# Kernel optimization log

Hardware: AMD Instinct MI355X
Metric: run time of the kernel (lower is better)

## Reference

```python
import jax, jax.numpy as jnp
import numpy as np

D_MODEL = 512
NHEAD = 8
HEAD_DIM = D_MODEL // NHEAD
SEQ = 4096
BATCH = 2
BASE = 10000.0


def rope_cache(seq_len, dim):
    inv_freq = 1.0 / (BASE ** (jnp.arange(0, dim, 2, dtype=jnp.float32) / dim))
    t = jnp.arange(seq_len, dtype=jnp.float32)
    freqs = jnp.einsum('i,j->ij', t, inv_freq)          # [S, dim/2]
    emb = jnp.concatenate([freqs, freqs], axis=-1)       # [S, dim]
    return jnp.cos(emb), jnp.sin(emb)


def rotate_half(x):
    h = x.shape[-1] // 2
    return jnp.concatenate([-x[..., h:], x[..., :h]], axis=-1)


def setup_inputs() -> dict:
    key = jax.random.key(0)
    ks = jax.random.split(key, 9)
    s = 1.0 / np.sqrt(D_MODEL)
    x = jax.random.normal(ks[0], (BATCH, SEQ, D_MODEL), dtype=jnp.float32)
    Wq = jax.random.uniform(ks[1], (D_MODEL, D_MODEL), jnp.float32, -s, s)
    bq = jax.random.uniform(ks[2], (D_MODEL,), jnp.float32, -s, s)
    Wk = jax.random.uniform(ks[3], (D_MODEL, D_MODEL), jnp.float32, -s, s)
    bk = jax.random.uniform(ks[4], (D_MODEL,), jnp.float32, -s, s)
    Wv = jax.random.uniform(ks[5], (D_MODEL, D_MODEL), jnp.float32, -s, s)
    bv = jax.random.uniform(ks[6], (D_MODEL,), jnp.float32, -s, s)
    Wo = jax.random.uniform(ks[7], (D_MODEL, D_MODEL), jnp.float32, -s, s)
    bo = jax.random.uniform(ks[8], (D_MODEL,), jnp.float32, -s, s)
    # causal mask: True where attention is disallowed (j > i)
    mask = jnp.triu(jnp.ones((SEQ, SEQ), dtype=bool), k=1)
    return {"x": x, "mask": mask, "Wq": Wq, "bq": bq, "Wk": Wk, "bk": bk,
            "Wv": Wv, "bv": bv, "Wo": Wo, "bo": bo}


def reference(x, mask, Wq, bq, Wk, bk, Wv, bv, Wo, bo):
    B, S, _ = x.shape
    def proj(W, b):
        y = x @ W.T + b
        return y.reshape(B, S, NHEAD, HEAD_DIM).transpose(0, 2, 1, 3)  # [B,H,S,D]
    q = proj(Wq, bq)
    k = proj(Wk, bk)
    v = proj(Wv, bv)
    cos, sin = rope_cache(S, HEAD_DIM)                    # [S, D]
    cos = cos[None, None]; sin = sin[None, None]
    q = q * cos + rotate_half(q) * sin
    k = k * cos + rotate_half(k) * sin
    scale = HEAD_DIM ** -0.5
    attn = jnp.einsum('bhid,bhjd->bhij', q, k) * scale    # [B,H,S,S]
    attn = jnp.where(mask[None, None], -jnp.inf, attn)
    attn = jax.nn.softmax(attn, axis=-1)
    out = jnp.einsum('bhij,bhjd->bhid', attn, v)          # [B,H,S,D]
    out = out.transpose(0, 2, 1, 3).reshape(B, S, D_MODEL)
    return out @ Wo.T + bo
```

## Files before the change

### kernel.cpp

```cpp
#include <hip/hip_runtime.h>
#include <hip/hip_bf16.h>

#define SEQLEN 4096
#define DMODEL 512
#define NHEADS 8

typedef short short8 __attribute__((ext_vector_type(8)));
typedef float f32x4  __attribute__((ext_vector_type(4)));
typedef float f32x16 __attribute__((ext_vector_type(16)));
typedef int   int2v  __attribute__((ext_vector_type(2)));

__device__ __forceinline__ unsigned short f2bf(float f) {
    union { float f; unsigned u; } v; v.f = f;
    unsigned r = v.u + 0x7fffu + ((v.u >> 16) & 1u);
    return (unsigned short)(r >> 16);
}
__device__ __forceinline__ float bf2f(unsigned short u) {
    union { unsigned u; float f; } v; v.u = (unsigned)u << 16; return v.f;
}
__device__ __forceinline__ float exp2v(float x) {
    float r; asm("v_exp_f32 %0, %1" : "=v"(r) : "v"(x)); return r;
}
__device__ __forceinline__ unsigned cvtpk(float lo, float hi) {
    unsigned r; asm("v_cvt_pk_bf16_f32 %0, %1, %2" : "=v"(r) : "v"(lo), "v"(hi)); return r;
}
__device__ __forceinline__ int2v pl32(int a, int b) {
    return __builtin_amdgcn_permlane32_swap(a, b, false, false);
}
__device__ __forceinline__ void gload16(const void* g, void* l) {
    __builtin_amdgcn_global_load_lds(
        (const __attribute__((address_space(1))) void*)g,
        (__attribute__((address_space(3))) void*)l, 16, 0, 0);
}
__device__ __forceinline__ int nchunks(int qs) { return (4 * qs + 4 + 9) / 10; }

__global__ __launch_bounds__(256)
void prep_kernel(const float* __restrict__ x,
                 const float* __restrict__ Wq, const float* __restrict__ Wk,
                 const float* __restrict__ Wv, const float* __restrict__ Wo,
                 unsigned short* __restrict__ xb, unsigned short* __restrict__ Wcat,
                 float* __restrict__ ct, float* __restrict__ st) {
    const int gid = blockIdx.x, tid = threadIdx.x;
    if (gid < 4096) {
        int i = gid * 1024 + tid * 4;
        float4 v = *reinterpret_cast<const float4*>(x + i);
        ushort4 o; o.x = f2bf(v.x); o.y = f2bf(v.y); o.z = f2bf(v.z); o.w = f2bf(v.w);
        *reinterpret_cast<ushort4*>(xb + i) = o;
    } else if (gid < 5120) {
        int i = (gid - 4096) * 1024 + tid * 4;
        int z = i >> 18;
        const float* W = (z == 0) ? Wq : (z == 1) ? Wk : (z == 2) ? Wv : Wo;
        int j = i & 262143;
        float4 v = *reinterpret_cast<const float4*>(W + j);
        ushort4 o; o.x = f2bf(v.x); o.y = f2bf(v.y); o.z = f2bf(v.z); o.w = f2bf(v.w);
        *reinterpret_cast<ushort4*>(Wcat + i) = o;
    } else {
        int idx = (gid - 5120) * 256 + tid;
        int s = idx >> 5, f = idx & 31;
        float inv = exp2f((float)f * -0.4152410118609203f);
        float a = (float)s * inv;
        ct[idx] = cosf(a); st[idx] = sinf(a);
    }
}

template<int MODE>
__global__ __launch_bounds__(256)
void gemm_kernel(const unsigned short* __restrict__ A,
                 const unsigned short* __restrict__ W,
                 const float* __restrict__ bq,
                 const float* __restrict__ bk,
                 const float* __restrict__ bv,
                 const float* __restrict__ ctab,
                 const float* __restrict__ stab,
                 unsigned short* __restrict__ Qb,
                 unsigned short* __restrict__ Kb,
                 unsigned short* __restrict__ Vt,
                 float* __restrict__ Fout)
{
    constexpr int K = 512;
    constexpr int BN  = (MODE == 0) ? 128 : 64;
    constexpr int NT  = (MODE == 0) ? 12 : 8;
    constexpr int CPX = (MODE == 0) ? 96 : 64;
    constexpr int NTF = (MODE == 0) ? 4 : 2;
    __shared__ __align__(16) unsigned short a_sh[3][128 * 32];
    __shared__ __align__(16) unsigned short b_sh[3][BN * 32];

    const int raw = blockIdx.x;
    const int bid = (raw & 7) * CPX + (raw >> 3);
    const int bm = bid / NT, bn = bid % NT;
    const int tid = threadIdx.x;
    const int w = tid >> 6, l = tid & 63;
    const int g = l >> 4, l15 = l & 15;
    const int wr = w >> 1, wc = w & 1;

    const int sr0 = tid >> 2;
    const int swzc = (tid & 3) ^ ((sr0 >> 1) & 3);
    const unsigned wbase = (unsigned)(tid & 0xC0) * 16;
    const unsigned short* arow = A + (size_t)(bm * 128 + sr0) * K + swzc * 8;
    const unsigned short* brow = W + (size_t)(bn * BN + sr0) * K + swzc * 8;

    f32x4 acc[4][NTF];
    #pragma unroll
    for (int p = 0; p < 4; ++p)
        #pragma unroll
        for (int q = 0; q < NTF; ++q)
            acc[p][q] = (f32x4){0.f, 0.f, 0.f, 0.f};

    auto stage = [&](int buf, int k0) {
        char* ab = (char*)a_sh[buf];
        char* bb2 = (char*)b_sh[buf];
        gload16(arow + k0,                      ab + wbase);
        gload16(arow + (size_t)64 * K + k0,     ab + 4096 + wbase);
        gload16(brow + k0,                      bb2 + wbase);
        if constexpr (MODE == 0)
            gload16(brow + (size_t)64 * K + k0, bb2 + 4096 + wbase);
    };
    auto waitvm = [&]() {
        if constexpr (MODE == 0) asm volatile("s_waitcnt vmcnt(4)" ::: "memory");
        else                     asm volatile("s_waitcnt vmcnt(3)" ::: "memory");
    };

    stage(0, 0);
    stage(1, 32);
    waitvm();
    __builtin_amdgcn_s_barrier();

    int cb = 0;
    for (int ks = 0; ks < 16; ++ks) {
        int pb = cb + 2; if (pb >= 3) pb -= 3;
        stage(pb, (ks + 2 < 16) ? (ks + 2) * 32 : 480);

        const char* ab = (const char*)a_sh[cb];
        const char* bb2 = (const char*)b_sh[cb];
        short8 af[4], bf[NTF];
        #pragma unroll
        for (int mt = 0; mt < 4; ++mt) {
            int r = wr * 64 + mt * 16 + l15;
            int ofs = (r * 64 + g * 16) ^ (((r >> 1) & 3) << 4);
            af[mt] = *reinterpret_cast<const short8*>(ab + ofs);
        }
        #pragma unroll
        for (int nt = 0; nt < NTF; ++nt) {
            int r = wc * (BN / 2) + nt * 16 + l15;
            int ofs = (r * 64 + g * 16) ^ (((r >> 1) & 3) << 4);
            bf[nt] = *reinterpret_cast<const short8*>(bb2 + ofs);
        }
        __builtin_amdgcn_s_setprio(1);
        #pragma unroll
        for (int mt = 0; mt < 4; ++mt)
            #pragma unroll
            for (int nt = 0; nt < NTF; ++nt)
                acc[mt][nt] = __builtin_amdgcn_mfma_f32_16x16x32_bf16(af[mt], bf[nt], acc[mt][nt], 0, 0, 0);
        __builtin_amdgcn_s_setprio(0);

        waitvm();
        __builtin_amdgcn_s_barrier();
        cb = (cb == 2) ? 0 : cb + 1;
    }

    const int m_base = bm * 128 + wr * 64;

    if (MODE == 1) {
        const int n_base = bn * 64 + wc * 32;
        #pragma unroll
        for (int mt = 0; mt < 4; ++mt)
            for (int nt = 0; nt < NTF; ++nt) {
                int n = n_base + nt * 16 + l15;
                float bb = bq[n];
                #pragma unroll
                for (int i = 0; i < 4; ++i) {
                    int m = m_base + mt * 16 + g * 4 + i;
                    Fout[(size_t)m * 512 + n] = acc[mt][nt][i] + bb;
                }
            }
    } else {
        const int z = bn >> 2;
        const int nc0 = (bn & 3) * 128 + wc * 64;
        const float* bias = (z == 0) ? bq : (z == 1) ? bk : bv;
        if (z < 2) {
            unsigned short* Y = z ? Kb : Qb;
            const float qsc = z ? 1.0f : 0.18033688011112042f;
            #pragma unroll
            for (int mt = 0; mt < 4; ++mt)
                for (int ntl = 0; ntl < 2; ++ntl) {
                    int hd0 = (ntl * 16 + l15) & 31;
                    int n0 = nc0 + ntl * 16 + l15;
                    float bb0 = bias[n0];
                    float bb1 = bias[n0 + 32];
                    #pragma unroll
                    for (int i = 0; i < 4; ++i) {
                        int m = m_base + mt * 16 + g * 4 + i;
                        int sidx = m & (SEQLEN - 1);
                        float cs = ctab[sidx * 32 + hd0];
                        float sn = stab[sidx * 32 + hd0];
                        float v0 = acc[mt][ntl][i] + bb0;
                        float v1 = acc[mt][ntl + 2][i] + bb1;
                        Y[(size_t)m * 512 + n0]      = f2bf((v0 * cs - v1 * sn) * qsc);
                        Y[(size_t)m * 512 + n0 + 32] = f2bf((v1 * cs + v0 * sn) * qsc);
                    }
                }
        } else if constexpr (MODE == 0) {
            asm volatile("s_waitcnt vmcnt(0)" ::: "memory");
            __builtin_amdgcn_s_barrier();
            char* T = (char*)a_sh;
            #pragma unroll
            for (int mt = 0; mt < 4; ++mt)
                #pragma unroll
                for (int nt = 0; nt < 4; ++nt) {
                    int nv_l = wc * 64 + nt * 16 + l15;
                    float bb = bias[(bn & 3) * 128 + nv_l];
                    #pragma unroll
                    for (int i = 0; i < 4; i += 2) {
                        int m_l = wr * 64 + mt * 16 + g * 4 + i;
                        unsigned u = cvtpk(acc[mt][nt][i] + bb, acc[mt][nt][i + 1] + bb);
                        int byte0 = nv_l * 256 + ((m_l * 2) ^ ((nv_l & 7) << 4));
                        *reinterpret_cast<unsigned*>(T + byte0) = u;
                    }
                }
            __builtin_amdgcn_s_barrier();
            const int b_out = bm >> 5;
            const int s0 = (bm & 31) * 128;
            #pragma unroll
            for (int p = 0; p < 8; ++p) {
                int nv_l = p * 16 + (tid >> 4);
                int c = tid & 15;
                int byte = nv_l * 256 + ((c * 16) ^ ((nv_l & 7) << 4));
                short8 v = *reinterpret_cast<const short8*>(T + byte);
                int nv_g = (bn & 3) * 128 + nv_l;
                int hg = nv_g >> 6, d = nv_g & 63;
                *reinterpret_cast<short8*>(
                    Vt + ((size_t)((b_out * 8 + hg) * 64 + d)) * SEQLEN + s0 + c * 8) = v;
            }
        }
    }
}

__global__ __launch_bounds__(256, 2)
void attn_kernel(const unsigned short* __restrict__ Qg,
                 const unsigned short* __restrict__ Kg,
                 const unsigned short* __restrict__ Vt,
                 unsigned short* __restrict__ O,
                 unsigned short* __restrict__ Opt,
                 float* __restrict__ Ml)
{
    __shared__ __align__(16) unsigned short k_sh[3][64 * 64];
    __shared__ __align__(16) unsigned short v_sh[3][64 * 64];

    const int bx = blockIdx.x;
    const int bh = bx & 15;
    const int idx = bx >> 4;
    int qs = 15, accn = 0;
    for (;;) {
        int nb = nchunks(qs);
        if (accn + nb > idx) break;
        accn += nb; --qs;
    }
    const int ck = idx - accn;
    const int HT4 = 4 * qs + 4;
    const int t0 = ck * 10;
    const int t1 = (t0 + 10 < HT4) ? t0 + 10 : HT4;
    const bool single = (HT4 <= 10);
    const int slot = bh * 61 + idx;

    const int b = bh >> 3, hh = bh & 7;
    const int tid = threadIdx.x;
    const int w = tid >> 6, l = tid & 63;
    const int l31 = l & 31, h = l >> 5;

    const size_t qkbase = (size_t)b * SEQLEN * DMODEL + hh * 64;
    const unsigned short* Vrow = Vt + (size_t)bh * 64 * SEQLEN;

    const int r0 = tid >> 3, cb0 = tid & 7;
    const int scs = cb0 ^ (r0 & 7);
    const unsigned short* ksrc0 = Kg + qkbase + (size_t)r0 * DMODEL + scs * 8;
    const unsigned short* vsrc0 = Vrow + (size_t)r0 * SEQLEN + scs * 8;

    const int swz = (l31 & 7) << 4;
    const int td = 4 * qs + w;
    const int tlimit = td + 1;
    const int qg0 = qs * 256 + w * 64 + l31;
    const int qg1 = qg0 + 32;
    const int ql0 = w * 64 + l31;
    const int ql1 = ql0 + 32;

    short8 qf0[4], qf1[4];
    {
        const unsigned short* qr0 = Qg + qkbase + (size_t)qg0 * DMODEL;
        const unsigned short* qr1 = Qg + qkbase + (size_t)qg1 * DMODEL;
        #pragma unroll
        for (int kk = 0; kk < 4; ++kk) {
            qf0[kk] = *reinterpret_cast<const short8*>(qr0 + kk * 16 + h * 8);
            qf1[kk] = *reinterpret_cast<const short8*>(qr1 + kk * 16 + h * 8);
        }
    }

    f32x16 oa00, oa01, oa10, oa11;
    #pragma unroll
    for (int i = 0; i < 16; ++i) { oa00[i] = 0.f; oa01[i] = 0.f; oa10[i] = 0.f; oa11[i] = 0.f; }
    float m0 = -3.0e38f, l0 = 0.f, m1 = -3.0e38f, l1 = 0.f;

    auto stage = [&](int buf, int t) {
        char* kb = (char*)k_sh[buf];
        char* vb = (char*)v_sh[buf];
        const unsigned short* kp = ksrc0 + (size_t)t * 64 * DMODEL;
        const unsigned short* vp = vsrc0 + t * 64;
        gload16(kp,                kb + tid * 16);
        gload16(kp + 32 * DMODEL,  kb + 4096 + tid * 16);
        gload16(vp,                vb + tid * 16);
        gload16(vp + 32 * SEQLEN,  vb + 4096 + tid * 16);
    };

    auto softmax_set = [&](f32x16& sA, f32x16& sB, float& mr, float& lr,
                           f32x16& oaA, f32x16& oaB, short8* pw) {
        float g0 = fmaxf(sA[0], sA[1]);
        g0 = fmaxf(fmaxf(g0, sA[2]), sA[3]);
        g0 = fmaxf(fmaxf(g0, sA[4]), sA[5]);
        g0 = fmaxf(fmaxf(g0, sA[6]), sA[7]);
        float g1 = fmaxf(sA[8], sA[9]);
        g1 = fmaxf(fmaxf(g1, sA[10]), sA[11]);
        g1 = fmaxf(fmaxf(g1, sA[12]), sA[13]);
        g1 = fmaxf(fmaxf(g1, sA[14]), sA[15]);
        float g2 = fmaxf(sB[0], sB[1]);
        g2 = fmaxf(fmaxf(g2, sB[2]), sB[3]);
        g2 = fmaxf(fmaxf(g2, sB[4]), sB[5]);
        g2 = fmaxf(fmaxf(g2, sB[6]), sB[7]);
        float g3 = fmaxf(sB[8], sB[9]);
        g3 = fmaxf(fmaxf(g3, sB[10]), sB[11]);
        g3 = fmaxf(fmaxf(g3, sB[12]), sB[13]);
        g3 = fmaxf(fmaxf(g3, sB[14]), sB[15]);
        float mloc = fmaxf(fmaxf(g0, g1), fmaxf(g2, g3));
        int2v rp2 = pl32(__float_as_int(mloc), __float_as_int(mloc));
        float pm = fmaxf(__int_as_float(rp2[0]), __int_as_float(rp2[1]));
        float mn = mr;
        if (__any(pm > mr + 8.0f)) {
            mn = fmaxf(mr, pm);
            float al = exp2v(mr - mn);
            mr = mn; lr *= al;
            #pragma unroll
            for (int r = 0; r < 16; ++r) { oaA[r] *= al; oaB[r] *= al; }
        }
        #pragma unroll
        for (int r = 0; r < 16; ++r) sA[r] = exp2v(sA[r] - mn);
        #pragma unroll
        for (int r = 0; r < 16; ++r) sB[r] = exp2v(sB[r] - mn);
        float sm[16];
        #pragma unroll
        for (int r = 0; r < 16; ++r) sm[r] = sA[r] + sB[r];
        #pragma unroll
        for (int str = 8; str >= 1; str >>= 1)
            #pragma unroll
            for (int r = 0; r < str; ++r) sm[r] += sm[r + str];
        int2v rs2 = pl32(__float_as_int(sm[0]), __float_as_int(sm[0]));
        lr += __int_as_float(rs2[0]) + __int_as_float(rs2[1]);
        #pragma unroll
        for (int bb = 0; bb < 4; ++bb) {
            const int rb = (bb & 1) * 8;
            const f32x16& s = (bb < 2) ? sA : sB;
            int pk0 = (int)cvtpk(s[rb + 0], s[rb + 1]);
            int pk1 = (int)cvtpk(s[rb + 2], s[rb + 3]);
            int pk2 = (int)cvtpk(s[rb + 4], s[rb + 5]);
            int pk3 = (int)cvtpk(s[rb + 6], s[rb + 7]);
            int2v r02 = pl32(pk0, pk2);
            int2v r13 = pl32(pk1, pk3);
            union { int u[4]; short8 s8; } w_;
            w_.u[0] = r02[0]; w_.u[1] = r13[0]; w_.u[2] = r02[1]; w_.u[3] = r13[1];
            pw[bb] = w_.s8;
        }
    };

    int cb = t0 % 3;
    stage(cb, t0);
    {
        int nb = cb + 1; if (nb >= 3) nb -= 3;
        stage(nb, (t0 + 1 < t1) ? t0 + 1 : t1 - 1);
    }
    asm volatile("s_waitcnt vmcnt(4)" ::: "memory");
    __builtin_amdgcn_s_barrier();

    for (int t = t0; t < t1; ++t) {
        int pb = cb + 2; if (pb >= 3) pb -= 3;
        stage(pb, (t + 2 < t1) ? t + 2 : t1 - 1);

        if (t < tlimit) {
            const char* kb = (const char*)k_sh[cb];
            const char* vb = (const char*)v_sh[cb];

            f32x16 s00, s01, s10, s11;
            #pragma unroll
            for (int i = 0; i < 16; ++i) { s00[i] = 0.f; s01[i] = 0.f; s10[i] = 0.f; s11[i] = 0.f; }
            __builtin_amdgcn_s_setprio(1);
            #pragma unroll
            for (int kk = 0; kk < 4; ++kk) {
                short8 kf0 = *reinterpret_cast<const short8*>(kb + l31 * 128 + ((kk * 32 + h * 16) ^ swz));
                short8 kf1 = *reinterpret_cast<const short8*>(kb + (32 + l31) * 128 + ((kk * 32 + h * 16) ^ swz));
                s00 = __builtin_amdgcn_mfma_f32_32x32x16_bf16(kf0, qf0[kk], s00, 0, 0, 0);
                s01 = __builtin_amdgcn_mfma_f32_32x32x16_bf16(kf1, qf0[kk], s01, 0, 0, 0);
                s10 = __builtin_amdgcn_mfma_f32_32x32x16_bf16(kf0, qf1[kk], s10, 0, 0, 0);
                s11 = __builtin_amdgcn_mfma_f32_32x32x16_bf16(kf1, qf1[kk], s11, 0, 0, 0);
            }
            __builtin_amdgcn_s_setprio(0);

            if (t == td) {
                #pragma unroll
                for (int r = 0; r < 16; ++r) {
                    int rp = (r & 3) + 8 * (r >> 2) + 4 * h;
                    int kv0 = t * 64 + rp;
                    if (kv0 > qg0)      s00[r] = -3.0e38f;
                    if (kv0 + 32 > qg0) s01[r] = -3.0e38f;
                    if (kv0 > qg1)      s10[r] = -3.0e38f;
                    if (kv0 + 32 > qg1) s11[r] = -3.0e38f;
                }
            }

            short8 pw0[4], pw1[4];
            softmax_set(s00, s01, m0, l0, oa00, oa01, pw0);
            softmax_set(s10, s11, m1, l1, oa10, oa11, pw1);

            __builtin_amdgcn_s_setprio(1);
            #pragma unroll
            for (int bb = 0; bb < 4; ++bb) {
                short8 vf0 = *reinterpret_cast<const short8*>(vb + l31 * 128 + ((bb * 32 + h * 16) ^ swz));
                short8 vf1 = *reinterpret_cast<const short8*>(vb + (32 + l31) * 128 + ((bb * 32 + h * 16) ^ swz));
                oa00 = __builtin_amdgcn_mfma_f32_32x32x16_bf16(vf0, pw0[bb], oa00, 0, 0, 0);
                oa01 = __builtin_amdgcn_mfma_f32_32x32x16_bf16(vf1, pw0[bb], oa01, 0, 0, 0);
                oa10 = __builtin_amdgcn_mfma_f32_32x32x16_bf16(vf0, pw1[bb], oa10, 0, 0, 0);
                oa11 = __builtin_amdgcn_mfma_f32_32x32x16_bf16(vf1, pw1[bb], oa11, 0, 0, 0);
            }
            __builtin_amdgcn_s_setprio(0);
        }

        asm volatile("s_waitcnt vmcnt(4)" ::: "memory");
        __builtin_amdgcn_s_barrier();
        cb = (cb == 2) ? 0 : cb + 1;
    }

    if (single) {
        float inv0 = 1.0f / l0, inv1 = 1.0f / l1;
        unsigned short* or0 = O + qkbase + (size_t)qg0 * DMODEL;
        unsigned short* or1 = O + qkbase + (size_t)qg1 * DMODEL;
        #pragma unroll
        for (int r = 0; r < 16; r += 2) {
            int d0 = (r & 3) + 8 * (r >> 2) + 4 * h;
            *reinterpret_cast<unsigned*>(or0 + d0)      = cvtpk(oa00[r] * inv0, oa00[r + 1] * inv0);
            *reinterpret_cast<unsigned*>(or0 + 32 + d0) = cvtpk(oa01[r] * inv0, oa01[r + 1] * inv0);
            *reinterpret_cast<unsigned*>(or1 + d0)      = cvtpk(oa10[r] * inv1, oa10[r + 1] * inv1);
            *reinterpret_cast<unsigned*>(or1 + 32 + d0) = cvtpk(oa11[r] * inv1, oa11[r + 1] * inv1);
        }
    } else {
        float* mlb = Ml + (size_t)slot * 512;
        *reinterpret_cast<float2*>(mlb + ql0 * 2) = make_float2(m0, l0);
        *reinterpret_cast<float2*>(mlb + ql1 * 2) = make_float2(m1, l1);
        unsigned short* opb = Opt + (size_t)slot * 16384;
        #pragma unroll
        for (int r = 0; r < 16; r += 2) {
            int d0 = (r & 3) + 8 * (r >> 2) + 4 * h;
            unsigned u;
            u = cvtpk(oa00[r], oa00[r + 1]);
            opb[d0 * 256 + ql0]        = (unsigned short)u;
            opb[(d0 + 1) * 256 + ql0]  = (unsigned short)(u >> 16);
            u = cvtpk(oa01[r], oa01[r + 1]);
            opb[(d0 + 32) * 256 + ql0] = (unsigned short)u;
            opb[(d0 + 33) * 256 + ql0] = (unsigned short)(u >> 16);
            u = cvtpk(oa10[r], oa10[r + 1]);
            opb[d0 * 256 + ql1]        = (unsigned short)u;
            opb[(d0 + 1) * 256 + ql1]  = (unsigned short)(u >> 16);
            u = cvtpk(oa11[r], oa11[r + 1]);
            opb[(d0 + 32) * 256 + ql1] = (unsigned short)u;
            opb[(d0 + 33) * 256 + ql1] = (unsigned short)(u >> 16);
        }
    }
}

__global__ __launch_bounds__(256)
void combine_kernel(const unsigned short* __restrict__ Opt, const float* __restrict__ Ml,
                    unsigned short* __restrict__ O) {
    __shared__ float a_sh[7][64];
    __shared__ unsigned short o_sh[64][72];
    const int bx = blockIdx.x;
    const int qs = 2 + (bx >> 6);
    const int rem = bx & 63;
    const int bh = rem >> 2, qq = rem & 3;
    const int b = bh >> 3, hh = bh & 7;
    const int tid = threadIdx.x;

    int accn = 0;
    for (int q2 = 15; q2 > qs; --q2) accn += nchunks(q2);
    const int nb = nchunks(qs);
    const int slotbase = bh * 61 + accn;

    if (tid < 64) {
        int q = qq * 64 + tid;
        float m = -3.0e38f;
        for (int c = 0; c < nb; ++c)
            m = fmaxf(m, Ml[(size_t)(slotbase + c) * 512 + q * 2]);
        float denom = 0.f;
        for (int c = 0; c < nb; ++c) {
            float2 ml = *reinterpret_cast<const float2*>(Ml + (size_t)(slotbase + c) * 512 + q * 2);
            float a = exp2v(ml.x - m);
            denom += a * ml.y;
            a_sh[c][tid] = a;
        }
        float inv = 1.0f / denom;
        for (int c = 0; c < nb; ++c) a_sh[c][tid] *= inv;
    }
    __syncthreads();

    const int d = tid >> 2, q4 = (tid & 3) * 16;
    float acc16[16];
    #pragma unroll
    for (int e = 0; e < 16; ++e) acc16[e] = 0.f;
    for (int c = 0; c < nb; ++c) {
        const unsigned short* p = Opt + (size_t)(slotbase + c) * 16384 + d * 256 + qq * 64 + q4;
        short8 v0 = *reinterpret_cast<const short8*>(p);
        short8 v1 = *reinterpret_cast<const short8*>(p + 8);
        #pragma unroll
        for (int e = 0; e < 8; ++e) {
            acc16[e]     += a_sh[c][q4 + e]     * bf2f((unsigned short)v0[e]);
            acc16[8 + e] += a_sh[c][q4 + 8 + e] * bf2f((unsigned short)v1[e]);
        }
    }
    #pragma unroll
    for (int e = 0; e < 16; ++e) o_sh[q4 + e][d] = f2bf(acc16[e]);
    __syncthreads();

    const int qw = tid >> 2, dc = (tid & 3) * 16;
    const int qglob = qs * 256 + qq * 64 + qw;
    unsigned short* orow = O + ((size_t)(b * 4096 + qglob)) * 512 + hh * 64 + dc;
    #pragma unroll
    for (int j = 0; j < 2; ++j) {
        union { ushort4 h4[2]; short8 s8; } u;
        u.h4[0] = *reinterpret_cast<const ushort4*>(&o_sh[qw][dc + j * 8]);
        u.h4[1] = *reinterpret_cast<const ushort4*>(&o_sh[qw][dc + j * 8 + 4]);
        *reinterpret_cast<short8*>(orow + j * 8) = u.s8;
    }
}

extern "C" void kernel_launch(void* const* d_in, const int* in_sizes, int n_in,
                              void* d_out, int out_size, void* d_ws, size_t ws_size,
                              hipStream_t stream) {
    const float* x  = (const float*)d_in[0];
    const float* Wq = (const float*)d_in[2];
    const float* bq = (const float*)d_in[3];
    const float* Wk = (const float*)d_in[4];
    const float* bk = (const float*)d_in[5];
    const float* Wv = (const float*)d_in[6];
    const float* bv = (const float*)d_in[7];
    const float* Wo = (const float*)d_in[8];
    const float* bo = (const float*)d_in[9];
    float* out = (float*)d_out;

    const int MD = 8192 * 512;
    const int WD = 512 * 512;
    unsigned short* ws  = (unsigned short*)d_ws;
    unsigned short* xb  = ws;
    unsigned short* Qb  = xb + MD;
    unsigned short* Kb  = Qb + MD;
    unsigned short* Vt  = Kb + MD;
    unsigned short* Ob  = Vt + MD;
    unsigned short* Wcat = Ob + MD;
    float* ctab = (float*)(Wcat + 4 * WD);
    float* stab = ctab + SEQLEN * 32;
    unsigned short* Opt = (unsigned short*)((char*)d_ws + 45088768ull);
    float* Ml  = (float*)((char*)d_ws + 45088768ull + 31981568ull);

    prep_kernel<<<5632, 256, 0, stream>>>(x, Wq, Wk, Wv, Wo, xb, Wcat, ctab, stab);

    gemm_kernel<0><<<dim3(64 * 12), 256, 0, stream>>>(
        xb, Wcat, bq, bk, bv, ctab, stab, Qb, Kb, Vt, nullptr);

    attn_kernel<<<dim3(976), 256, 0, stream>>>(Qb, Kb, Vt, Ob, Opt, Ml);
    combine_kernel<<<dim3(896), 256, 0, stream>>>(Opt, Ml, Ob);

    gemm_kernel<1><<<dim3(64 * 8), 256, 0, stream>>>(
        Ob, Wcat + 3 * WD, bo, nullptr, nullptr, nullptr, nullptr,
        nullptr, nullptr, nullptr, out);
}
```

Baseline: 219.5 us.

## Load V fragments directly from global, drop V LDS staging, split attention launch

V tiles are no longer staged through shared memory. Each lane now loads its V fragments straight from global memory into registers after the QK MFMAs, which halves LDS use and the wait counts. Launch bounds rise to 3 blocks per SM to use the freed LDS. The attention grid is split into two launches through an index offset. The direct V loads are not prefetched, so global latency is exposed inside the loop, and the extra launch adds overhead.

```diff
diff --git a/kernel.cpp b/kernel.cpp
--- a/kernel.cpp
+++ b/kernel.cpp
@@ -235,20 +235,20 @@
     }
 }
 
-__global__ __launch_bounds__(256, 2)
+__global__ __launch_bounds__(256, 3)
 void attn_kernel(const unsigned short* __restrict__ Qg,
                  const unsigned short* __restrict__ Kg,
                  const unsigned short* __restrict__ Vt,
                  unsigned short* __restrict__ O,
                  unsigned short* __restrict__ Opt,
-                 float* __restrict__ Ml)
+                 float* __restrict__ Ml,
+                 int idx_off)
 {
     __shared__ __align__(16) unsigned short k_sh[3][64 * 64];
-    __shared__ __align__(16) unsigned short v_sh[3][64 * 64];
 
     const int bx = blockIdx.x;
     const int bh = bx & 15;
-    const int idx = bx >> 4;
+    const int idx = (bx >> 4) + idx_off;
     int qs = 15, accn = 0;
     for (;;) {
         int nb = nchunks(qs);
@@ -273,7 +273,8 @@
     const int r0 = tid >> 3, cb0 = tid & 7;
     const int scs = cb0 ^ (r0 & 7);
     const unsigned short* ksrc0 = Kg + qkbase + (size_t)r0 * DMODEL + scs * 8;
-    const unsigned short* vsrc0 = Vrow + (size_t)r0 * SEQLEN + scs * 8;
+    const unsigned short* vrow0 = Vrow + (size_t)l31 * SEQLEN + h * 8;
+    const unsigned short* vrow1 = Vrow + (size_t)(32 + l31) * SEQLEN + h * 8;
 
     const int swz = (l31 & 7) << 4;
     const int td = 4 * qs + w;
@@ -301,13 +302,9 @@
 
     auto stage = [&](int buf, int t) {
         char* kb = (char*)k_sh[buf];
-        char* vb = (char*)v_sh[buf];
         const unsigned short* kp = ksrc0 + (size_t)t * 64 * DMODEL;
-        const unsigned short* vp = vsrc0 + t * 64;
         gload16(kp,                kb + tid * 16);
         gload16(kp + 32 * DMODEL,  kb + 4096 + tid * 16);
-        gload16(vp,                vb + tid * 16);
-        gload16(vp + 32 * SEQLEN,  vb + 4096 + tid * 16);
     };
 
     auto softmax_set = [&](f32x16& sA, f32x16& sB, float& mr, float& lr,
@@ -374,7 +371,7 @@
         int nb = cb + 1; if (nb >= 3) nb -= 3;
         stage(nb, (t0 + 1 < t1) ? t0 + 1 : t1 - 1);
     }
-    asm volatile("s_waitcnt vmcnt(4)" ::: "memory");
+    asm volatile("s_waitcnt vmcnt(2)" ::: "memory");
     __builtin_amdgcn_s_barrier();
 
     for (int t = t0; t < t1; ++t) {
@@ -383,7 +380,6 @@
 
         if (t < tlimit) {
             const char* kb = (const char*)k_sh[cb];
-            const char* vb = (const char*)v_sh[cb];
 
             f32x16 s00, s01, s10, s11;
             #pragma unroll
@@ -399,6 +395,13 @@
                 s11 = __builtin_amdgcn_mfma_f32_32x32x16_bf16(kf1, qf1[kk], s11, 0, 0, 0);
             }
             __builtin_amdgcn_s_setprio(0);
+
+            short8 vf0[4], vf1[4];
+            #pragma unroll
+            for (int bb = 0; bb < 4; ++bb) {
+                vf0[bb] = *reinterpret_cast<const short8*>(vrow0 + t * 64 + bb * 16);
+                vf1[bb] = *reinterpret_cast<const short8*>(vrow1 + t * 64 + bb * 16);
+            }
 
             if (t == td) {
                 #pragma unroll
@@ -419,17 +422,15 @@
             __builtin_amdgcn_s_setprio(1);
             #pragma unroll
             for (int bb = 0; bb < 4; ++bb) {
-                short8 vf0 = *reinterpret_cast<const short8*>(vb + l31 * 128 + ((bb * 32 + h * 16) ^ swz));
-                short8 vf1 = *reinterpret_cast<const short8*>(vb + (32 + l31) * 128 + ((bb * 32 + h * 16) ^ swz));
-                oa00 = __builtin_amdgcn_mfma_f32_32x32x16_bf16(vf0, pw0[bb], oa00, 0, 0, 0);
-                oa01 = __builtin_amdgcn_mfma_f32_32x32x16_bf16(vf1, pw0[bb], oa01, 0, 0, 0);
-                oa10 = __builtin_amdgcn_mfma_f32_32x32x16_bf16(vf0, pw1[bb], oa10, 0, 0, 0);
-                oa11 = __builtin_amdgcn_mfma_f32_32x32x16_bf16(vf1, pw1[bb], oa11, 0, 0, 0);
+                oa00 = __builtin_amdgcn_mfma_f32_32x32x16_bf16(vf0[bb], pw0[bb], oa00, 0, 0, 0);
+                oa01 = __builtin_amdgcn_mfma_f32_32x32x16_bf16(vf1[bb], pw0[bb], oa01, 0, 0, 0);
+                oa10 = __builtin_amdgcn_mfma_f32_32x32x16_bf16(vf0[bb], pw1[bb], oa10, 0, 0, 0);
+                oa11 = __builtin_amdgcn_mfma_f32_32x32x16_bf16(vf1[bb], pw1[bb], oa11, 0, 0, 0);
             }
             __builtin_amdgcn_s_setprio(0);
         }
 
-        asm volatile("s_waitcnt vmcnt(4)" ::: "memory");
+        asm volatile("s_waitcnt vmcnt(2)" ::: "memory");
         __builtin_amdgcn_s_barrier();
         cb = (cb == 2) ? 0 : cb + 1;
     }
@@ -568,7 +569,9 @@
     gemm_kernel<0><<<dim3(64 * 12), 256, 0, stream>>>(
         xb, Wcat, bq, bk, bv, ctab, stab, Qb, Kb, Vt, nullptr);
 
-    attn_kernel<<<dim3(976), 256, 0, stream>>>(Qb, Kb, Vt, Ob, Opt, Ml);
+    attn_kernel<<<dim3(30 * 16), 256, 0, stream>>>(Qb, Kb, Vt, Ob, Opt, Ml, 0);
+    attn_kernel<<<dim3(31 * 16), 256, 0, stream>>>(Qb, Kb, Vt, Ob, Opt, Ml, 30);
+
     combine_kernel<<<dim3(896), 256, 0, stream>>>(Opt, Ml, Ob);
 
     gemm_kernel<1><<<dim3(64 * 8), 256, 0, stream>>>(
```

Result: slower. 332.1 us (+51.3%).
